# Performance work log

Measured on AMD Instinct MI355X. Metric: run time of the kernel, lower is better.

Reference implementation:

```python
import jax, jax.numpy as jnp
import numpy as np
import math

TIME_DIM = 32

def fourier_time_embedding(t, time_dim=TIME_DIM):
    # Sinusoidal Fourier features of scalar t -> [time_dim]
    half = time_dim // 2
    freqs = jnp.exp(-math.log(10000.0) * jnp.arange(half, dtype=jnp.float32) / half)
    args = t * freqs
    return jnp.concatenate([jnp.sin(args), jnp.cos(args)], axis=-1)


def setup_inputs() -> dict:
    key = jax.random.key(0)
    kh, ka, kw1, kb1, kw2, kb2 = jax.random.split(key, 6)
    B, C, D, T = 16, 1024, 256, 9
    h0 = jax.random.normal(kh, (B, C, D), dtype=jnp.float32)
    time_grid = jnp.arange(T, dtype=jnp.float32)
    adjacency = jax.random.uniform(ka, (B, C, C), dtype=jnp.float32)
    in_dim = 2 * D + TIME_DIM  # 544
    s1 = 1.0 / math.sqrt(in_dim)
    s2 = 1.0 / math.sqrt(D)
    W1 = jax.random.uniform(kw1, (in_dim, D), jnp.float32, -s1, s1)
    b1 = jax.random.uniform(kb1, (D,), jnp.float32, -s1, s1)
    W2 = jax.random.uniform(kw2, (D, D), jnp.float32, -s2, s2)
    b2 = jax.random.uniform(kb2, (D,), jnp.float32, -s2, s2)
    return {"h0": h0, "time_grid": time_grid, "adjacency": adjacency,
            "W1": W1, "b1": b1, "W2": W2, "b2": b2}


def reference(h0, time_grid, adjacency, W1, b1, W2, b2):
    B, C, D = h0.shape
    # adjacency is [B,C,C] (time-constant branch); degree-normalize once
    degree = jnp.clip(adjacency.sum(-1, keepdims=True), 1.0, None)
    adj_norm = adjacency / degree

    def vector_field(t, h):
        agg = jnp.einsum('bij,bjd->bid', adj_norm, h)           # [B,C,D]
        te = fourier_time_embedding(t)                           # [TIME_DIM]
        te_b = jnp.broadcast_to(te, (B, C, TIME_DIM))
        x = jnp.concatenate([h, agg, te_b], axis=-1)             # [B,C,2D+time]
        return jnp.tanh(x @ W1 + b1) @ W2 + b2                   # [B,C,D]

    def rk4_step(h, ts):
        t0, t1 = ts
        dt = t1 - t0
        k1 = vector_field(t0, h)
        k2 = vector_field(t0 + dt / 2, h + dt * k1 / 2)
        k3 = vector_field(t0 + dt / 2, h + dt * k2 / 2)
        k4 = vector_field(t0 + dt, h + dt * k3)
        h_new = h + dt * (k1 + 2 * k2 + 2 * k3 + k4) / 6
        return h_new, h_new

    ts_pairs = jnp.stack([time_grid[:-1], time_grid[1:]], axis=-1)  # [T-1,2]
    _, states = jax.lax.scan(rk4_step, h0, ts_pairs)                 # [T-1,B,C,D]
    traj = jnp.concatenate([h0[None], states], axis=0)               # [T,B,C,D]
    return jnp.transpose(traj, (1, 0, 2, 3))                         # [B,T,C,D]
```

## Files before the change

### kernel.cpp

```cpp
#include <hip/hip_runtime.h>
#include <math.h>

#define NB   16
#define NC   1024
#define ND   256
#define NT_  9
#define TDIM 32

typedef _Float16 half8 __attribute__((ext_vector_type(8)));
typedef _Float16 half4v __attribute__((ext_vector_type(4)));
typedef float f32x4 __attribute__((ext_vector_type(4)));

#define GLL(gp, lp)                                                            \
  __builtin_amdgcn_global_load_lds(                                            \
      (const __attribute__((address_space(1))) void*)(gp),                     \
      (__attribute__((address_space(3))) void*)(lp), 16, 0, 0)

#define GLL4(gp, lp)                                                           \
  __builtin_amdgcn_global_load_lds(                                            \
      (const __attribute__((address_space(1))) void*)(gp),                     \
      (__attribute__((address_space(3))) void*)(lp), 4, 0, 0)

#define MFMA16(A, B, C) __builtin_amdgcn_mfma_f32_16x16x32_f16(A, B, C, 0, 0, 0)

#define VBAR(N)                                                                \
  do {                                                                         \
    asm volatile("s_waitcnt vmcnt(" #N ")" ::: "memory");                      \
    __builtin_amdgcn_s_barrier();                                              \
    asm volatile("" ::: "memory");                                             \
    __builtin_amdgcn_sched_barrier(0);                                         \
  } while (0)

#define BAR2()                                                                 \
  do {                                                                         \
    asm volatile("" ::: "memory");                                             \
    __builtin_amdgcn_s_barrier();                                              \
    asm volatile("" ::: "memory");                                             \
  } while (0)

#define LBAR()                                                                 \
  do {                                                                         \
    asm volatile("s_waitcnt lgkmcnt(0)" ::: "memory");                         \
    __builtin_amdgcn_s_barrier();                                              \
    asm volatile("" ::: "memory");                                             \
    __builtin_amdgcn_sched_barrier(0);                                         \
  } while (0)


__global__ __launch_bounds__(256) void k_copy_h0(const float* __restrict__ h0,
                                                 float* __restrict__ out) {
  size_t idx = (size_t)blockIdx.x * blockDim.x + threadIdx.x;
  size_t fe = idx * 4;
  size_t b = fe / ((size_t)NC * ND);
  size_t rem = fe % ((size_t)NC * ND);
  float4 v = *(const float4*)(h0 + fe);
  *(float4*)(out + (b * NT_) * (size_t)NC * ND + rem) = v;
}

__global__ __launch_bounds__(256) void k_deg(const float* __restrict__ adj,
                                             float* __restrict__ invdeg) {
  int wave = threadIdx.x >> 6;
  int lane = threadIdx.x & 63;
  int row = blockIdx.x * 4 + wave;
  const float* p = adj + (size_t)row * NC;
  float s = 0.f;
#pragma unroll
  for (int q = 0; q < 4; ++q) {
    float4 v = *(const float4*)(p + q * 256 + lane * 4);
    s += v.x + v.y + v.z + v.w;
  }
#pragma unroll
  for (int off = 32; off; off >>= 1) s += __shfl_down(s, off);
  if (lane == 0) invdeg[row] = 1.f / fmaxf(s, 1.f);
}

__global__ __launch_bounds__(256) void k_split_adj(const float* __restrict__ adj,
                                                   _Float16* __restrict__ adjT) {
  int i = blockIdx.x * 256 + threadIdx.x;
  int k0 = (i & 255) * 4;
  int c = (i >> 8) & 1023;
  int b = i >> 18;
  float4 v = *(const float4*)(adj + (((size_t)b * NC + c) << 10) + k0);
  half4v h;
  h[0] = (_Float16)v.x; h[1] = (_Float16)v.y;
  h[2] = (_Float16)v.z; h[3] = (_Float16)v.w;
  int mq = c >> 5, t = k0 >> 5;
  size_t base = ((((size_t)b * 32 + mq) * 32) + t) * 1024;
  int chunk = ((k0 & 31) >> 3) * 32 + (c & 31);
  *(half4v*)(adjT + base + chunk * 8 + (k0 & 7)) = h;
}

__global__ __launch_bounds__(256) void k_split_w(const float* __restrict__ W1,
                                                 const float* __restrict__ W2,
                                                 _Float16* __restrict__ W1Tt,
                                                 _Float16* __restrict__ W2Tt) {
  int blk = blockIdx.x;
  int tid = threadIdx.x;
  if (blk < 128) {
    int i = blk * 256 + tid;
    int n = i & 255, k0 = (i >> 8) * 4;
    half4v h;
#pragma unroll
    for (int q = 0; q < 4; ++q) h[q] = (_Float16)W1[(size_t)(k0 + q) * ND + n];
    int t = k0 >> 5;
    int chunk = ((k0 & 31) >> 3) * 256 + n;
    *(half4v*)(W1Tt + (size_t)t * 8192 + chunk * 8 + (k0 & 7)) = h;
  } else {
    int i = (blk - 128) * 256 + tid;
    int n = i & 255, k0 = (i >> 8) * 4;
    half4v h;
#pragma unroll
    for (int q = 0; q < 4; ++q) h[q] = (_Float16)W2[(size_t)(k0 + q) * ND + n];
    int t = k0 >> 5;
    int chunk = ((k0 & 31) >> 3) * 256 + n;
    *(half4v*)(W2Tt + (size_t)t * 8192 + chunk * 8 + (k0 & 7)) = h;
  }
}

__global__ __launch_bounds__(256) void k_htsplit(const float* __restrict__ src,
                                                 _Float16* __restrict__ hHt,
                                                 _Float16* __restrict__ hLt,
                                                 _Float16* __restrict__ hTt) {
  int i = blockIdx.x * 256 + threadIdx.x;
  int d0 = (i & 63) * 4;
  int c = (i >> 6) & 1023;
  int b = i >> 16;
  float4 v = *(const float4*)(src + (((size_t)b * NC + c) << 8) + d0);
  float vv[4] = {v.x, v.y, v.z, v.w};
  half4v hh, ll;
#pragma unroll
  for (int q = 0; q < 4; ++q) {
    _Float16 h = (_Float16)vv[q];
    hh[q] = h;
    ll[q] = (_Float16)(vv[q] - (float)h);
  }
  int mq = c >> 5, ta = d0 >> 5;
  size_t abase = ((((size_t)b * 32 + mq) * 8) + ta) * 1024;
  int achunk = ((d0 & 31) >> 3) * 32 + (c & 31);
  *(half4v*)(hHt + abase + achunk * 8 + (d0 & 7)) = hh;
  *(half4v*)(hLt + abase + achunk * 8 + (d0 & 7)) = ll;
  size_t tbase = ((size_t)b * 32 + mq) * 8192;
  int gk = (c & 31) >> 3, offc = c & 7;
#pragma unroll
  for (int q = 0; q < 4; ++q)
    hTt[tbase + (size_t)(gk * 256 + d0 + q) * 8 + offc] = hh[q];
}

__global__ __launch_bounds__(512, 4) void k_stage(
    const _Float16* __restrict__ adjT,
    _Float16* __restrict__ hHt, _Float16* __restrict__ hLt,
    const _Float16* __restrict__ hTr, _Float16* __restrict__ hTw,
    const float* __restrict__ invdeg,
    const _Float16* __restrict__ W1Tt, const _Float16* __restrict__ W2Tt,
    const float* __restrict__ W1, const float* __restrict__ b1,
    const float* __restrict__ b2, const float* __restrict__ tg,
    int step, int stage, float* __restrict__ out, float* __restrict__ accws) {
  __shared__ __align__(16) _Float16 Bs3[3][8192];
  __shared__ __align__(16) _Float16 As3[3][2048];
  __shared__ __align__(16) _Float16 POOL[8192];
  __shared__ float te_s[TDIM];
  __shared__ float b1s[256];
  _Float16* aggS = POOL;
  _Float16* uS = POOL;

  const int tid = threadIdx.x;
  const int lane = tid & 63, wid = tid >> 6;
  const int g = lane >> 4, r = lane & 15, rg = (lane >> 4) * 4;
  const int p = blockIdx.x;
  const int b = ((p >> 3) >> 5) * 8 + (p & 7);
  const int mq = (p >> 3) & 31;

  const _Float16* adjB = adjT + (((size_t)b * 32 + mq) * 32) * 1024;
  const _Float16* hTb = hTr + (size_t)b * 32 * 8192;
  const _Float16* hHb = hHt + (((size_t)b * 32 + mq) * 8) * 1024;
  const _Float16* hLb = hLt + (((size_t)b * 32 + mq) * 8) * 1024;

  f32x4 acc[2][2] = {};

  float iv[2][4];
#pragma unroll
  for (int i = 0; i < 2; ++i)
#pragma unroll
    for (int q = 0; q < 4; ++q)
      iv[i][q] = invdeg[b * NC + mq * 32 + i * 16 + rg + q];

#define STAGE_B(SRC, DST)                                                      \
  do {                                                                         \
    GLL((SRC) + (size_t)tid * 8, (DST) + (size_t)tid * 8);                     \
    GLL((SRC) + (size_t)(512 + tid) * 8, (DST) + (size_t)(512 + tid) * 8);     \
  } while (0)

  auto issue = [&](int S2) {
    if (S2 < 32) {
      GLL4(adjB + (size_t)S2 * 1024 + tid * 2, As3[S2 % 3] + (size_t)tid * 2);
      STAGE_B(hTb + (size_t)S2 * 8192, Bs3[S2 % 3]);
    } else if (S2 < 48) {
      int ta = S2 - 32;
      if (ta < 8) {
        GLL4(hHb + (size_t)ta * 1024 + tid * 2, As3[S2 % 3] + (size_t)tid * 2);
        GLL4(hLb + (size_t)ta * 1024 + tid * 2,
             As3[S2 % 3] + 1024 + (size_t)tid * 2);
      }
      STAGE_B(W1Tt + (size_t)ta * 8192, Bs3[S2 % 3]);
    } else if (S2 < 56) {
      STAGE_B(W2Tt + (size_t)(S2 - 48) * 8192, Bs3[S2 % 3]);
    }
  };

  issue(0);
  issue(1);
  if (tid < 16) {
    float t0 = tg[step], t1 = tg[step + 1];
    float frac = (stage == 0) ? 0.f : ((stage == 3) ? 1.f : 0.5f);
    float t = t0 + frac * (t1 - t0);
    float f = expf(-logf(10000.f) * (float)tid / 16.f);
    te_s[tid] = sinf(t * f);
    te_s[tid + 16] = cosf(t * f);
  }
  LBAR();
  if (tid < 256) {
    float s = b1[tid];
#pragma unroll
    for (int q = 0; q < TDIM; ++q)
      s = fmaf(te_s[q], W1[(size_t)(512 + q) * ND + tid], s);
    b1s[tid] = s;
  }

  for (int t = 0; t < 32; ++t) {
    int cur = t % 3;
    issue(t + 2);
    if (t < 30) VBAR(6);
    else if (t == 30) VBAR(7);
    else VBAR(8);
    half8 Af[2], Bf[2];
#pragma unroll
    for (int i = 0; i < 2; ++i)
      Af[i] = ((const half8*)As3[cur])[g * 32 + i * 16 + r];
#pragma unroll
    for (int j = 0; j < 2; ++j)
      Bf[j] = ((const half8*)Bs3[cur])[g * 256 + wid * 32 + j * 16 + r];
#pragma unroll
    for (int i = 0; i < 2; ++i)
#pragma unroll
      for (int j = 0; j < 2; ++j) acc[i][j] = MFMA16(Af[i], Bf[j], acc[i][j]);
    BAR2();
  }
#pragma unroll
  for (int i = 0; i < 2; ++i) {
#pragma unroll
    for (int j = 0; j < 2; ++j) {
      int d = wid * 32 + j * 16 + r;
#pragma unroll
      for (int q = 0; q < 4; ++q) {
        int lr = i * 16 + rg + q;
        float v = acc[i][j][q] * iv[i][q];
        aggS[((d >> 3) * 32 + lr) * 8 + (d & 7)] = (_Float16)v;
      }
      acc[i][j] = (f32x4){0.f, 0.f, 0.f, 0.f};
    }
  }
  LBAR();

  for (int ta = 0; ta < 16; ++ta) {
    int S = 32 + ta;
    int cur = S % 3;
    issue(S + 2);
    if (ta < 6) VBAR(8);
    else if (ta == 6) VBAR(6);
    else VBAR(4);
    half8 AH[2], AL[2], Bf[2];
    const bool hasL = (ta < 8);
    if (hasL) {
#pragma unroll
      for (int i = 0; i < 2; ++i) {
        AH[i] = ((const half8*)As3[cur])[g * 32 + i * 16 + r];
        AL[i] = ((const half8*)(As3[cur] + 1024))[g * 32 + i * 16 + r];
      }
    } else {
#pragma unroll
      for (int i = 0; i < 2; ++i)
        AH[i] = ((const half8*)aggS)[((ta - 8) * 4 + g) * 32 + i * 16 + r];
    }
#pragma unroll
    for (int j = 0; j < 2; ++j)
      Bf[j] = ((const half8*)Bs3[cur])[g * 256 + wid * 32 + j * 16 + r];
#pragma unroll
    for (int i = 0; i < 2; ++i)
#pragma unroll
      for (int j = 0; j < 2; ++j) {
        acc[i][j] = MFMA16(AH[i], Bf[j], acc[i][j]);
        if (hasL) acc[i][j] = MFMA16(AL[i], Bf[j], acc[i][j]);
      }
    BAR2();
  }
#pragma unroll
  for (int i = 0; i < 2; ++i) {
#pragma unroll
    for (int j = 0; j < 2; ++j) {
      int col = wid * 32 + j * 16 + r;
#pragma unroll
      for (int q = 0; q < 4; ++q) {
        int row = i * 16 + rg + q;
        float v = tanhf(acc[i][j][q] + b1s[col]);
        uS[((col >> 3) * 32 + row) * 8 + (col & 7)] = (_Float16)v;
      }
      acc[i][j] = (f32x4){0.f, 0.f, 0.f, 0.f};
    }
  }
  LBAR();

  for (int tb = 0; tb < 8; ++tb) {
    int S = 48 + tb;
    int cur = S % 3;
    issue(S + 2);
    if (tb < 6) VBAR(4);
    else if (tb == 6) VBAR(2);
    else VBAR(0);
    half8 Af[2], Bf[2];
#pragma unroll
    for (int i = 0; i < 2; ++i)
      Af[i] = ((const half8*)uS)[(tb * 4 + g) * 32 + i * 16 + r];
#pragma unroll
    for (int j = 0; j < 2; ++j)
      Bf[j] = ((const half8*)Bs3[cur])[g * 256 + wid * 32 + j * 16 + r];
#pragma unroll
    for (int i = 0; i < 2; ++i)
#pragma unroll
      for (int j = 0; j < 2; ++j) acc[i][j] = MFMA16(Af[i], Bf[j], acc[i][j]);
    BAR2();
  }
  const float t0 = tg[step], t1 = tg[step + 1];
  const float dt = t1 - t0;
  const float cs = (stage == 2) ? dt : 0.5f * dt;
#pragma unroll
  for (int i = 0; i < 2; ++i) {
#pragma unroll
    for (int j = 0; j < 2; ++j) {
      int col = wid * 32 + j * 16 + r;
      float bb2 = b2[col];
      int ii0 = mq * 32 + i * 16 + rg;
      size_t hrow = (((size_t)b * NT_ + step) * NC + ii0) * (size_t)ND + col;
      size_t wrow = ((size_t)b * NC + ii0) * (size_t)ND + col;
      float val[4];
#pragma unroll
      for (int q = 0; q < 4; ++q) {
        float f = acc[i][j][q] + bb2;
        float hb = out[hrow + (size_t)q * ND];
        size_t widx = wrow + (size_t)q * ND;
        if (stage == 0) {
          accws[widx] = f;
          val[q] = hb + cs * f;
        } else if (stage == 3) {
          float hn = hb + (dt / 6.f) * (accws[widx] + f);
          out[hrow + (size_t)NC * ND + (size_t)q * ND] = hn;
          val[q] = hn;
        } else {
          accws[widx] += 2.f * f;
          val[q] = hb + cs * f;
        }
      }
      half4v th, tl;
#pragma unroll
      for (int q = 0; q < 4; ++q) {
        _Float16 hh = (_Float16)val[q];
        th[q] = hh;
        tl[q] = (_Float16)(val[q] - (float)hh);
      }
      int ta = col >> 5;
      size_t hbase = (((size_t)b * 32 + mq) * 8 + ta) * 1024;
      int cb = ((col & 31) >> 3) * 32 + (ii0 & 31);
      int offc = col & 7;
#pragma unroll
      for (int q = 0; q < 4; ++q) {
        hHt[hbase + (size_t)(cb + q) * 8 + offc] = th[q];
        hLt[hbase + (size_t)(cb + q) * 8 + offc] = tl[q];
      }
      size_t tbase = ((size_t)b * 32 + mq) * 8192;
      int gk = (ii0 & 31) >> 3;
      *(half4v*)(hTw + tbase + (size_t)(gk * 256 + col) * 8 + (ii0 & 7)) = th;
    }
  }
#undef STAGE_B
}

extern "C" void kernel_launch(void* const* d_in, const int* in_sizes, int n_in,
                              void* d_out, int out_size, void* d_ws, size_t ws_size,
                              hipStream_t stream) {
  const float* h0 = (const float*)d_in[0];
  const float* tg = (const float*)d_in[1];
  const float* adj = (const float*)d_in[2];
  const float* W1 = (const float*)d_in[3];
  const float* b1 = (const float*)d_in[4];
  const float* W2 = (const float*)d_in[5];
  const float* b2 = (const float*)d_in[6];
  float* out = (float*)d_out;

  const size_t CD = (size_t)NC * ND;
  char* w = (char*)d_ws;
  float* invdeg = (float*)w;     w += (size_t)16384 * 4;
  float* accws = (float*)w;      w += (size_t)NB * CD * 4;
  _Float16* adjT = (_Float16*)w; w += (size_t)NB * NC * NC * 2;
  _Float16* hHt = (_Float16*)w;  w += (size_t)NB * CD * 2;
  _Float16* hLt = (_Float16*)w;  w += (size_t)NB * CD * 2;
  _Float16* hTa = (_Float16*)w;  w += (size_t)NB * CD * 2;
  _Float16* hTb = (_Float16*)w;  w += (size_t)NB * CD * 2;
  _Float16* W1Tt = (_Float16*)w; w += (size_t)256 * 512 * 2;
  _Float16* W2Tt = (_Float16*)w; w += (size_t)256 * 256 * 2;

  k_copy_h0<<<dim3(4096), dim3(256), 0, stream>>>(h0, out);
  k_deg<<<dim3(4096), dim3(256), 0, stream>>>(adj, invdeg);
  k_split_adj<<<dim3(16384), dim3(256), 0, stream>>>(adj, adjT);
  k_split_w<<<dim3(192), dim3(256), 0, stream>>>(W1, W2, W1Tt, W2Tt);
  k_htsplit<<<dim3(4096), dim3(256), 0, stream>>>(h0, hHt, hLt, hTa);

  int par = 0;
  for (int s = 0; s < NT_ - 1; ++s) {
    for (int st = 0; st < 4; ++st) {
      k_stage<<<dim3(512), dim3(512), 0, stream>>>(
          adjT, hHt, hLt, par ? hTb : hTa, par ? hTa : hTb, invdeg, W1Tt, W2Tt,
          W1, b1, b2, tg, s, st, out, accws);
      par ^= 1;
    }
  }
}
```

Baseline: 1.571 ms.

## Double row tile to 64 per block, halving grid and reusing B tiles

Each workgroup now computes 64 rows instead of 32, with the 8 waves arranged 2x4 over rows and columns. Every wave holds a 2x4 set of accumulators, and the grid shrinks from 512 to 256 blocks. Each staged B tile (the h transpose, W1 and W2) is therefore reused across twice as many rows, which halves the global and LDS traffic for B. In exchange, shared memory per block grows, launch bounds drop to 2 blocks per CU, and only 256 blocks are launched. That may leave part of the MI355X's CUs underused.

```diff
diff --git a/kernel.cpp b/kernel.cpp
--- a/kernel.cpp
+++ b/kernel.cpp
@@ -146,7 +146,7 @@
     hTt[tbase + (size_t)(gk * 256 + d0 + q) * 8 + offc] = hh[q];
 }
 
-__global__ __launch_bounds__(512, 4) void k_stage(
+__global__ __launch_bounds__(512, 2) void k_stage(
     const _Float16* __restrict__ adjT,
     _Float16* __restrict__ hHt, _Float16* __restrict__ hLt,
     const _Float16* __restrict__ hTr, _Float16* __restrict__ hTw,
@@ -156,8 +156,8 @@
     const float* __restrict__ b2, const float* __restrict__ tg,
     int step, int stage, float* __restrict__ out, float* __restrict__ accws) {
   __shared__ __align__(16) _Float16 Bs3[3][8192];
-  __shared__ __align__(16) _Float16 As3[3][2048];
-  __shared__ __align__(16) _Float16 POOL[8192];
+  __shared__ __align__(16) _Float16 As3[3][4096];
+  __shared__ __align__(16) _Float16 POOL[16384];
   __shared__ float te_s[TDIM];
   __shared__ float b1s[256];
   _Float16* aggS = POOL;
@@ -165,24 +165,26 @@
 
   const int tid = threadIdx.x;
   const int lane = tid & 63, wid = tid >> 6;
+  const int wm = wid >> 2, wn = wid & 3;
   const int g = lane >> 4, r = lane & 15, rg = (lane >> 4) * 4;
   const int p = blockIdx.x;
-  const int b = ((p >> 3) >> 5) * 8 + (p & 7);
-  const int mq = (p >> 3) & 31;
-
-  const _Float16* adjB = adjT + (((size_t)b * 32 + mq) * 32) * 1024;
+  const int slot = p >> 3;
+  const int b = (slot >> 4) * 8 + (p & 7);
+  const int mq = slot & 15;
+
+  const _Float16* adjB = adjT + (((size_t)b * 32 + mq * 2) * 32) * 1024;
   const _Float16* hTb = hTr + (size_t)b * 32 * 8192;
-  const _Float16* hHb = hHt + (((size_t)b * 32 + mq) * 8) * 1024;
-  const _Float16* hLb = hLt + (((size_t)b * 32 + mq) * 8) * 1024;
-
-  f32x4 acc[2][2] = {};
+  const _Float16* hHb = hHt + ((size_t)b * 32 + mq * 2) * 8192;
+  const _Float16* hLb = hLt + ((size_t)b * 32 + mq * 2) * 8192;
+
+  f32x4 acc[2][4] = {};
 
   float iv[2][4];
 #pragma unroll
   for (int i = 0; i < 2; ++i)
 #pragma unroll
     for (int q = 0; q < 4; ++q)
-      iv[i][q] = invdeg[b * NC + mq * 32 + i * 16 + rg + q];
+      iv[i][q] = invdeg[b * NC + mq * 64 + wm * 32 + i * 16 + rg + q];
 
 #define STAGE_B(SRC, DST)                                                      \
   do {                                                                         \
@@ -192,14 +194,18 @@
 
   auto issue = [&](int S2) {
     if (S2 < 32) {
-      GLL4(adjB + (size_t)S2 * 1024 + tid * 2, As3[S2 % 3] + (size_t)tid * 2);
+      _Float16* d = As3[S2 % 3];
+      GLL4(adjB + (size_t)S2 * 1024 + tid * 2, d + (size_t)tid * 2);
+      GLL4(adjB + 32768 + (size_t)S2 * 1024 + tid * 2, d + 1024 + (size_t)tid * 2);
       STAGE_B(hTb + (size_t)S2 * 8192, Bs3[S2 % 3]);
     } else if (S2 < 48) {
       int ta = S2 - 32;
+      _Float16* d = As3[S2 % 3];
       if (ta < 8) {
-        GLL4(hHb + (size_t)ta * 1024 + tid * 2, As3[S2 % 3] + (size_t)tid * 2);
-        GLL4(hLb + (size_t)ta * 1024 + tid * 2,
-             As3[S2 % 3] + 1024 + (size_t)tid * 2);
+        GLL4(hHb + (size_t)ta * 1024 + tid * 2, d + (size_t)tid * 2);
+        GLL4(hHb + 8192 + (size_t)ta * 1024 + tid * 2, d + 1024 + (size_t)tid * 2);
+        GLL4(hLb + (size_t)ta * 1024 + tid * 2, d + 2048 + (size_t)tid * 2);
+        GLL4(hLb + 8192 + (size_t)ta * 1024 + tid * 2, d + 3072 + (size_t)tid * 2);
       }
       STAGE_B(W1Tt + (size_t)ta * 8192, Bs3[S2 % 3]);
     } else if (S2 < 56) {
@@ -229,32 +235,35 @@
   for (int t = 0; t < 32; ++t) {
     int cur = t % 3;
     issue(t + 2);
-    if (t < 30) VBAR(6);
-    else if (t == 30) VBAR(7);
-    else VBAR(8);
-    half8 Af[2], Bf[2];
+    if (t < 30) VBAR(8);
+    else if (t == 30) VBAR(10);
+    else VBAR(12);
+    half8 Af[2], Bf[4];
+#pragma unroll
+    for (int i = 0; i < 2; ++i) {
+      int row = wm * 32 + i * 16 + r;
+      Af[i] = ((const half8*)As3[cur])[(row >> 5) * 128 + g * 32 + (row & 31)];
+    }
+#pragma unroll
+    for (int j = 0; j < 4; ++j)
+      Bf[j] = ((const half8*)Bs3[cur])[g * 256 + wn * 64 + j * 16 + r];
 #pragma unroll
     for (int i = 0; i < 2; ++i)
-      Af[i] = ((const half8*)As3[cur])[g * 32 + i * 16 + r];
-#pragma unroll
-    for (int j = 0; j < 2; ++j)
-      Bf[j] = ((const half8*)Bs3[cur])[g * 256 + wid * 32 + j * 16 + r];
-#pragma unroll
-    for (int i = 0; i < 2; ++i)
-#pragma unroll
-      for (int j = 0; j < 2; ++j) acc[i][j] = MFMA16(Af[i], Bf[j], acc[i][j]);
+#pragma unroll
+      for (int j = 0; j < 4; ++j) acc[i][j] = MFMA16(Af[i], Bf[j], acc[i][j]);
     BAR2();
   }
 #pragma unroll
   for (int i = 0; i < 2; ++i) {
 #pragma unroll
-    for (int j = 0; j < 2; ++j) {
-      int d = wid * 32 + j * 16 + r;
+    for (int j = 0; j < 4; ++j) {
+      int d = wn * 64 + j * 16 + r;
 #pragma unroll
       for (int q = 0; q < 4; ++q) {
-        int lr = i * 16 + rg + q;
+        int r31 = i * 16 + rg + q;
         float v = acc[i][j][q] * iv[i][q];
-        aggS[((d >> 3) * 32 + lr) * 8 + (d & 7)] = (_Float16)v;
+        aggS[(size_t)(d >> 5) * 2048 + wm * 1024 +
+             (((d & 31) >> 3) * 32 + r31) * 8 + (d & 7)] = (_Float16)v;
       }
       acc[i][j] = (f32x4){0.f, 0.f, 0.f, 0.f};
     }
@@ -265,29 +274,34 @@
     int S = 32 + ta;
     int cur = S % 3;
     issue(S + 2);
-    if (ta < 6) VBAR(8);
-    else if (ta == 6) VBAR(6);
+    if (ta < 6) VBAR(12);
+    else if (ta == 6) VBAR(8);
     else VBAR(4);
-    half8 AH[2], AL[2], Bf[2];
+    half8 AH[2], AL[2], Bf[4];
     const bool hasL = (ta < 8);
     if (hasL) {
 #pragma unroll
       for (int i = 0; i < 2; ++i) {
-        AH[i] = ((const half8*)As3[cur])[g * 32 + i * 16 + r];
-        AL[i] = ((const half8*)(As3[cur] + 1024))[g * 32 + i * 16 + r];
+        int row = wm * 32 + i * 16 + r;
+        int ci = (row >> 5) * 128 + g * 32 + (row & 31);
+        AH[i] = ((const half8*)As3[cur])[ci];
+        AL[i] = ((const half8*)(As3[cur] + 2048))[ci];
       }
     } else {
 #pragma unroll
-      for (int i = 0; i < 2; ++i)
-        AH[i] = ((const half8*)aggS)[((ta - 8) * 4 + g) * 32 + i * 16 + r];
-    }
-#pragma unroll
-    for (int j = 0; j < 2; ++j)
-      Bf[j] = ((const half8*)Bs3[cur])[g * 256 + wid * 32 + j * 16 + r];
+      for (int i = 0; i < 2; ++i) {
+        int row = wm * 32 + i * 16 + r;
+        AH[i] = ((const half8*)aggS)[(ta - 8) * 256 + (row >> 5) * 128 + g * 32 +
+                                     (row & 31)];
+      }
+    }
+#pragma unroll
+    for (int j = 0; j < 4; ++j)
+      Bf[j] = ((const half8*)Bs3[cur])[g * 256 + wn * 64 + j * 16 + r];
 #pragma unroll
     for (int i = 0; i < 2; ++i)
 #pragma unroll
-      for (int j = 0; j < 2; ++j) {
+      for (int j = 0; j < 4; ++j) {
         acc[i][j] = MFMA16(AH[i], Bf[j], acc[i][j]);
         if (hasL) acc[i][j] = MFMA16(AL[i], Bf[j], acc[i][j]);
       }
@@ -296,13 +310,14 @@
 #pragma unroll
   for (int i = 0; i < 2; ++i) {
 #pragma unroll
-    for (int j = 0; j < 2; ++j) {
-      int col = wid * 32 + j * 16 + r;
+    for (int j = 0; j < 4; ++j) {
+      int col = wn * 64 + j * 16 + r;
 #pragma unroll
       for (int q = 0; q < 4; ++q) {
-        int row = i * 16 + rg + q;
+        int r31 = i * 16 + rg + q;
         float v = tanhf(acc[i][j][q] + b1s[col]);
-        uS[((col >> 3) * 32 + row) * 8 + (col & 7)] = (_Float16)v;
+        uS[(size_t)(col >> 5) * 2048 + wm * 1024 +
+           (((col & 31) >> 3) * 32 + r31) * 8 + (col & 7)] = (_Float16)v;
       }
       acc[i][j] = (f32x4){0.f, 0.f, 0.f, 0.f};
     }
@@ -316,17 +331,19 @@
     if (tb < 6) VBAR(4);
     else if (tb == 6) VBAR(2);
     else VBAR(0);
-    half8 Af[2], Bf[2];
+    half8 Af[2], Bf[4];
+#pragma unroll
+    for (int i = 0; i < 2; ++i) {
+      int row = wm * 32 + i * 16 + r;
+      Af[i] = ((const half8*)uS)[tb * 256 + (row >> 5) * 128 + g * 32 + (row & 31)];
+    }
+#pragma unroll
+    for (int j = 0; j < 4; ++j)
+      Bf[j] = ((const half8*)Bs3[cur])[g * 256 + wn * 64 + j * 16 + r];
 #pragma unroll
     for (int i = 0; i < 2; ++i)
-      Af[i] = ((const half8*)uS)[(tb * 4 + g) * 32 + i * 16 + r];
-#pragma unroll
-    for (int j = 0; j < 2; ++j)
-      Bf[j] = ((const half8*)Bs3[cur])[g * 256 + wid * 32 + j * 16 + r];
-#pragma unroll
-    for (int i = 0; i < 2; ++i)
-#pragma unroll
-      for (int j = 0; j < 2; ++j) acc[i][j] = MFMA16(Af[i], Bf[j], acc[i][j]);
+#pragma unroll
+      for (int j = 0; j < 4; ++j) acc[i][j] = MFMA16(Af[i], Bf[j], acc[i][j]);
     BAR2();
   }
   const float t0 = tg[step], t1 = tg[step + 1];
@@ -335,10 +352,10 @@
 #pragma unroll
   for (int i = 0; i < 2; ++i) {
 #pragma unroll
-    for (int j = 0; j < 2; ++j) {
-      int col = wid * 32 + j * 16 + r;
+    for (int j = 0; j < 4; ++j) {
+      int col = wn * 64 + j * 16 + r;
       float bb2 = b2[col];
-      int ii0 = mq * 32 + i * 16 + rg;
+      int ii0 = mq * 64 + wm * 32 + i * 16 + rg;
       size_t hrow = (((size_t)b * NT_ + step) * NC + ii0) * (size_t)ND + col;
       size_t wrow = ((size_t)b * NC + ii0) * (size_t)ND + col;
       float val[4];
@@ -367,7 +384,7 @@
         tl[q] = (_Float16)(val[q] - (float)hh);
       }
       int ta = col >> 5;
-      size_t hbase = (((size_t)b * 32 + mq) * 8 + ta) * 1024;
+      size_t hbase = (((size_t)b * 32 + (ii0 >> 5)) * 8 + ta) * 1024;
       int cb = ((col & 31) >> 3) * 32 + (ii0 & 31);
       int offc = col & 7;
 #pragma unroll
@@ -375,7 +392,7 @@
         hHt[hbase + (size_t)(cb + q) * 8 + offc] = th[q];
         hLt[hbase + (size_t)(cb + q) * 8 + offc] = tl[q];
       }
-      size_t tbase = ((size_t)b * 32 + mq) * 8192;
+      size_t tbase = ((size_t)b * 32 + (ii0 >> 5)) * 8192;
       int gk = (ii0 & 31) >> 3;
       *(half4v*)(hTw + tbase + (size_t)(gk * 256 + col) * 8 + (ii0 & 7)) = th;
     }
@@ -416,7 +433,7 @@
   int par = 0;
   for (int s = 0; s < NT_ - 1; ++s) {
     for (int st = 0; st < 4; ++st) {
-      k_stage<<<dim3(512), dim3(512), 0, stream>>>(
+      k_stage<<<dim3(256), dim3(512), 0, stream>>>(
           adjT, hHt, hLt, par ? hTb : hTa, par ? hTa : hTb, invdeg, W1Tt, W2Tt,
           W1, b1, b2, tg, s, st, out, accws);
       par ^= 1;
```

Result: slower. 1.880 ms (+19.7%).
